# Performance work log

Measured on AMD Instinct MI355X. Metric: run time of the kernel, lower is better.

The kernel has to match this reference:

```python
import jax, jax.numpy as jnp
import numpy as np

S, B, H2, M = 4096, 16, 1024, 4096  # seq_len, batch, 2*hidden_size, max_number_of_entries


def setup_inputs() -> dict:
    key = jax.random.key(0)
    ks = jax.random.split(key, 5)
    return {
        "encoder_outputs": jax.random.normal(ks[0], (S, B, H2), jnp.float32),
        "state": jax.random.normal(ks[1], (B, H2), jnp.float32),
        "previous_attention": jax.random.uniform(ks[2], (B, M), jnp.float32),
        "attn_w": jax.random.normal(ks[3], (H2, H2), jnp.float32) / np.sqrt(H2).astype(np.float32),
        "attn_b": jnp.zeros((H2,), jnp.float32),
        "time_w": jax.random.normal(ks[4], (M, M), jnp.float32) / np.sqrt(M).astype(np.float32),
        "time_b": jnp.zeros((M,), jnp.float32),
    }


def reference(encoder_outputs, state, previous_attention, attn_w, attn_b, time_w, time_b):
    # encoder_outputs: [S, B, 2H]; state: [B, 2H]; previous_attention: [B, M]
    seq_len = encoder_outputs.shape[0]
    # attend(): Linear on state, then per-timestep dot product with encoder output.
    # The original Python loop over S timesteps + torch.cat is one batched matvec:
    altered_state = state @ attn_w.T + attn_b                      # [B, 2H]
    weights = jnp.einsum('bd,sbd->bs', altered_state, encoder_outputs)  # [B, S]
    # time_attention branch (its result is computed but unused by the outputs,
    # mirrored here for faithfulness to the original forward)
    apw = previous_attention @ time_w.T + time_b                   # [B, M]
    prev_probs = jax.nn.softmax(apw[:, :seq_len], axis=0)          # softmax over batch dim, as in original
    _adjusted_weights = prev_probs * weights                       # dead value in the original module
    # final softmax attention + weighted sum over encoder outputs
    normalized_weights = jax.nn.softmax(weights, axis=1)           # [B, S]
    attention_applied = jnp.einsum('bs,sbd->bd', normalized_weights, encoder_outputs)  # [B, 2H]
    return attention_applied, normalized_weights
```

## Files before the change

kernel.cpp:

```cpp
#include <hip/hip_runtime.h>
#include <cstdint>
#include <cstddef>

#define S_LEN 4096
#define B_SZ 16
#define H2D 1024
#define CHUNKS 64
#define WPB 4
#define P_PER_B (CHUNKS * WPB)
#define S_PER_WAVE (S_LEN / P_PER_B)

__device__ __forceinline__ void load16(const float* __restrict__ p, float v[16]) {
    const float4* q = (const float4*)p;
    float4 x0 = q[0], x1 = q[1], x2 = q[2], x3 = q[3];
    v[0] = x0.x; v[1] = x0.y; v[2]  = x0.z; v[3]  = x0.w;
    v[4] = x1.x; v[5] = x1.y; v[6]  = x1.z; v[7]  = x1.w;
    v[8] = x2.x; v[9] = x2.y; v[10] = x2.z; v[11] = x2.w;
    v[12] = x3.x; v[13] = x3.y; v[14] = x3.z; v[15] = x3.w;
}

__global__ __launch_bounds__(256) void k_altered(const float* __restrict__ state,
                                                 const float* __restrict__ attn_w,
                                                 const float* __restrict__ attn_b,
                                                 float* __restrict__ altered) {
    const int i = (blockIdx.x * blockDim.x + threadIdx.x) >> 6;
    const int lane = threadIdx.x & 63;
    float r[16];
    load16(attn_w + (size_t)i * H2D + lane * 16, r);
    const float bias = attn_b[i];
    for (int b = 0; b < B_SZ; ++b) {
        float s[16];
        load16(state + b * H2D + lane * 16, s);
        float p = 0.f;
#pragma unroll
        for (int k = 0; k < 16; ++k) p += r[k] * s[k];
#pragma unroll
        for (int off = 32; off; off >>= 1) p += __shfl_xor(p, off, 64);
        if (lane == 0) altered[b * H2D + i] = p + bias;
    }
}

__global__ __launch_bounds__(256) void k_flash(const float* __restrict__ enc,
                                               const float* __restrict__ altered,
                                               float* __restrict__ w_raw,
                                               float* __restrict__ pm,
                                               float* __restrict__ pl,
                                               float* __restrict__ pacc) {
    const int b = blockIdx.y;
    const int wave = threadIdx.x >> 6;
    const int lane = threadIdx.x & 63;
    const int p_idx = blockIdx.x * WPB + wave;

    float a[16];
    load16(altered + b * H2D + lane * 16, a);

    float m = -1e30f, l = 0.f;
    float acc[16];
#pragma unroll
    for (int i = 0; i < 16; ++i) acc[i] = 0.f;

    const int s_start = blockIdx.x * (S_LEN / CHUNKS) + wave;

    for (int k = 0; k < S_PER_WAVE; k += 2) {
        const int sA = s_start + WPB * k;
        const int sB = sA + WPB;
        float eA[16], eB[16];
        load16(enc + ((size_t)sA * B_SZ + b) * H2D + lane * 16, eA);
        load16(enc + ((size_t)sB * B_SZ + b) * H2D + lane * 16, eB);
        float pA = 0.f, pB = 0.f;
#pragma unroll
        for (int i = 0; i < 16; ++i) { pA += a[i] * eA[i]; pB += a[i] * eB[i]; }
#pragma unroll
        for (int off = 32; off; off >>= 1) {
            pA += __shfl_xor(pA, off, 64);
            pB += __shfl_xor(pB, off, 64);
        }
        if (lane == 0) {
            w_raw[b * S_LEN + sA] = pA;
            w_raw[b * S_LEN + sB] = pB;
        }
        float mn = fmaxf(m, pA);
        float sc = __expf(m - mn);
        float ex = __expf(pA - mn);
        l = l * sc + ex;
#pragma unroll
        for (int i = 0; i < 16; ++i) acc[i] = acc[i] * sc + ex * eA[i];
        m = mn;
        mn = fmaxf(m, pB);
        sc = __expf(m - mn);
        ex = __expf(pB - mn);
        l = l * sc + ex;
#pragma unroll
        for (int i = 0; i < 16; ++i) acc[i] = acc[i] * sc + ex * eB[i];
        m = mn;
    }

    const size_t pi = (size_t)(b * P_PER_B + p_idx);
    if (lane == 0) { pm[pi] = m; pl[pi] = l; }
    float4* pa = (float4*)(pacc + pi * H2D + lane * 16);
    pa[0] = make_float4(acc[0],  acc[1],  acc[2],  acc[3]);
    pa[1] = make_float4(acc[4],  acc[5],  acc[6],  acc[7]);
    pa[2] = make_float4(acc[8],  acc[9],  acc[10], acc[11]);
    pa[3] = make_float4(acc[12], acc[13], acc[14], acc[15]);
}

__global__ __launch_bounds__(P_PER_B) void k_reduce(const float* __restrict__ pm,
                                                    const float* __restrict__ pl,
                                                    float* __restrict__ cexp,
                                                    float* __restrict__ MZ) {
    const int b = blockIdx.x, t = threadIdx.x;
    __shared__ float sm[P_PER_B];
    const float mv = pm[b * P_PER_B + t];
    sm[t] = mv;
    __syncthreads();
    for (int o = P_PER_B / 2; o; o >>= 1) {
        if (t < o) sm[t] = fmaxf(sm[t], sm[t + o]);
        __syncthreads();
    }
    const float M = sm[0];
    __syncthreads();
    const float e = __expf(mv - M);
    sm[t] = e * pl[b * P_PER_B + t];
    __syncthreads();
    for (int o = P_PER_B / 2; o; o >>= 1) {
        if (t < o) sm[t] += sm[t + o];
        __syncthreads();
    }
    cexp[b * P_PER_B + t] = e;
    if (t == 0) {
        MZ[b * 2]     = M;
        MZ[b * 2 + 1] = 1.f / sm[0];
    }
}

__global__ __launch_bounds__(64) void k_combine(const float* __restrict__ pacc,
                                                const float* __restrict__ cexp,
                                                const float* __restrict__ MZ,
                                                float* __restrict__ out_attn) {
    const int b = blockIdx.x >> 4;
    const int d = ((blockIdx.x & 15) << 6) + threadIdx.x;
    float sum = 0.f;
    const float* base = pacc + (size_t)b * P_PER_B * H2D + d;
    const float* c = cexp + b * P_PER_B;
#pragma unroll 8
    for (int p = 0; p < P_PER_B; ++p) {
        sum += c[p] * base[(size_t)p * H2D];
    }
    out_attn[b * H2D + d] = sum * MZ[b * 2 + 1];
}

__global__ __launch_bounds__(256) void k_norm(const float* __restrict__ w_raw,
                                              const float* __restrict__ MZ,
                                              float* __restrict__ out_nw) {
    const int idx = blockIdx.x * 256 + threadIdx.x;
    const int b = idx >> 12;
    out_nw[idx] = __expf(w_raw[idx] - MZ[b * 2]) * MZ[b * 2 + 1];
}

extern "C" void kernel_launch(void* const* d_in, const int* in_sizes, int n_in,
                              void* d_out, int out_size, void* d_ws, size_t ws_size,
                              hipStream_t stream) {
    const float* enc    = (const float*)d_in[0];
    const float* state  = (const float*)d_in[1];
    const float* attn_w = (const float*)d_in[3];
    const float* attn_b = (const float*)d_in[4];

    float* ws = (float*)d_ws;
    float* altered = ws;
    float* w_raw   = ws + 16384;
    float* pm      = ws + 81920;
    float* pl      = ws + 86016;
    float* cexp    = ws + 90112;
    float* MZ      = ws + 94208;
    float* pacc    = ws + 95232;

    float* out_attn = (float*)d_out;
    float* out_nw   = (float*)d_out + B_SZ * H2D;

    hipLaunchKernelGGL(k_altered, dim3(256), dim3(256), 0, stream,
                       state, attn_w, attn_b, altered);
    hipLaunchKernelGGL(k_flash, dim3(CHUNKS, B_SZ), dim3(256), 0, stream,
                       enc, altered, w_raw, pm, pl, pacc);
    hipLaunchKernelGGL(k_reduce, dim3(B_SZ), dim3(P_PER_B), 0, stream,
                       pm, pl, cexp, MZ);
    hipLaunchKernelGGL(k_combine, dim3(B_SZ * H2D / 64), dim3(64), 0, stream,
                       pacc, cexp, MZ, out_attn);
    hipLaunchKernelGGL(k_norm, dim3(B_SZ * S_LEN / 256), dim3(256), 0, stream,
                       w_raw, MZ, out_nw);
}
```

Baseline: 428.6 us.

## Replace single-pass online softmax with two-pass scores then weighted sum

Drops the fused online-softmax flash kernel in favor of a score pass, a standalone softmax, and a second pass over encoder outputs that accumulates with normalized weights, followed by a two-level reduction. It also switches loads to lane-strided float4 for coalescing and issues four rows per iteration. This removes the per-row exp and rescale work from the streaming loop but reads the 256MB encoder tensor twice, roughly doubling memory traffic.

```diff
diff --git a/kernel.cpp b/kernel.cpp
--- a/kernel.cpp
+++ b/kernel.cpp
@@ -5,156 +5,167 @@
 #define S_LEN 4096
 #define B_SZ 16
 #define H2D 1024
-#define CHUNKS 64
-#define WPB 4
-#define P_PER_B (CHUNKS * WPB)
-#define S_PER_WAVE (S_LEN / P_PER_B)
-
-__device__ __forceinline__ void load16(const float* __restrict__ p, float v[16]) {
-    const float4* q = (const float4*)p;
-    float4 x0 = q[0], x1 = q[1], x2 = q[2], x3 = q[3];
-    v[0] = x0.x; v[1] = x0.y; v[2]  = x0.z; v[3]  = x0.w;
-    v[4] = x1.x; v[5] = x1.y; v[6]  = x1.z; v[7]  = x1.w;
-    v[8] = x2.x; v[9] = x2.y; v[10] = x2.z; v[11] = x2.w;
-    v[12] = x3.x; v[13] = x3.y; v[14] = x3.z; v[15] = x3.w;
+#define P_PER_B 256
+
+__device__ __forceinline__ float dot4(float4 a, float4 b) {
+    return a.x * b.x + a.y * b.y + a.z * b.z + a.w * b.w;
+}
+__device__ __forceinline__ void axpy4(float4& acc, float w, float4 v) {
+    acc.x += w * v.x; acc.y += w * v.y; acc.z += w * v.z; acc.w += w * v.w;
 }
 
 __global__ __launch_bounds__(256) void k_altered(const float* __restrict__ state,
                                                  const float* __restrict__ attn_w,
                                                  const float* __restrict__ attn_b,
                                                  float* __restrict__ altered) {
-    const int i = (blockIdx.x * blockDim.x + threadIdx.x) >> 6;
+    const int i = (blockIdx.x * 256 + threadIdx.x) >> 6;
     const int lane = threadIdx.x & 63;
-    float r[16];
-    load16(attn_w + (size_t)i * H2D + lane * 16, r);
+    const float4* w4 = (const float4*)(attn_w + (size_t)i * H2D);
+    float4 r[4];
+#pragma unroll
+    for (int j = 0; j < 4; ++j) r[j] = w4[lane + 64 * j];
     const float bias = attn_b[i];
     for (int b = 0; b < B_SZ; ++b) {
-        float s[16];
-        load16(state + b * H2D + lane * 16, s);
+        const float4* s4 = (const float4*)(state + b * H2D);
         float p = 0.f;
 #pragma unroll
-        for (int k = 0; k < 16; ++k) p += r[k] * s[k];
+        for (int j = 0; j < 4; ++j) p += dot4(r[j], s4[lane + 64 * j]);
 #pragma unroll
         for (int off = 32; off; off >>= 1) p += __shfl_xor(p, off, 64);
         if (lane == 0) altered[b * H2D + i] = p + bias;
     }
 }
 
-__global__ __launch_bounds__(256) void k_flash(const float* __restrict__ enc,
+__global__ __launch_bounds__(256) void k_pass1(const float* __restrict__ enc,
                                                const float* __restrict__ altered,
-                                               float* __restrict__ w_raw,
-                                               float* __restrict__ pm,
-                                               float* __restrict__ pl,
+                                               float* __restrict__ w_raw) {
+    const int b = blockIdx.y;
+    const int wave = threadIdx.x >> 6, lane = threadIdx.x & 63;
+    const int slot = blockIdx.x * 4 + wave;
+    const float4* a4p = (const float4*)(altered + b * H2D);
+    float4 af[4];
+#pragma unroll
+    for (int j = 0; j < 4; ++j) af[j] = a4p[lane + 64 * j];
+    const int s0 = slot * 16;
+    for (int k = 0; k < 16; k += 4) {
+        float4 e[4][4];
+#pragma unroll
+        for (int r = 0; r < 4; ++r) {
+            const float4* e4 = (const float4*)(enc + ((size_t)(s0 + k + r) * B_SZ + b) * H2D);
+#pragma unroll
+            for (int j = 0; j < 4; ++j) e[r][j] = e4[lane + 64 * j];
+        }
+        float p[4];
+#pragma unroll
+        for (int r = 0; r < 4; ++r) {
+            p[r] = 0.f;
+#pragma unroll
+            for (int j = 0; j < 4; ++j) p[r] += dot4(af[j], e[r][j]);
+        }
+#pragma unroll
+        for (int off = 32; off; off >>= 1) {
+#pragma unroll
+            for (int r = 0; r < 4; ++r) p[r] += __shfl_xor(p[r], off, 64);
+        }
+        if (lane == 0) {
+#pragma unroll
+            for (int r = 0; r < 4; ++r) w_raw[b * S_LEN + s0 + k + r] = p[r];
+        }
+    }
+}
+
+__global__ __launch_bounds__(1024) void k_softmax(const float* __restrict__ w_raw,
+                                                  float* __restrict__ out_nw) {
+    const int b = blockIdx.x, t = threadIdx.x;
+    const int wave = t >> 6, lane = t & 63;
+    __shared__ float sm[16], ss[16], sbc[2];
+    float4 v = ((const float4*)(w_raw + b * S_LEN))[t];
+    float m = fmaxf(fmaxf(v.x, v.y), fmaxf(v.z, v.w));
+#pragma unroll
+    for (int off = 32; off; off >>= 1) m = fmaxf(m, __shfl_xor(m, off, 64));
+    if (lane == 0) sm[wave] = m;
+    __syncthreads();
+    if (t == 0) {
+        float M = sm[0];
+#pragma unroll
+        for (int i = 1; i < 16; ++i) M = fmaxf(M, sm[i]);
+        sbc[0] = M;
+    }
+    __syncthreads();
+    const float M = sbc[0];
+    float4 e;
+    e.x = __expf(v.x - M); e.y = __expf(v.y - M);
+    e.z = __expf(v.z - M); e.w = __expf(v.w - M);
+    float s = e.x + e.y + e.z + e.w;
+#pragma unroll
+    for (int off = 32; off; off >>= 1) s += __shfl_xor(s, off, 64);
+    if (lane == 0) ss[wave] = s;
+    __syncthreads();
+    if (t == 0) {
+        float Z = 0.f;
+#pragma unroll
+        for (int i = 0; i < 16; ++i) Z += ss[i];
+        sbc[1] = 1.f / Z;
+    }
+    __syncthreads();
+    const float iZ = sbc[1];
+    ((float4*)(out_nw + b * S_LEN))[t] = make_float4(e.x * iZ, e.y * iZ, e.z * iZ, e.w * iZ);
+}
+
+__global__ __launch_bounds__(256) void k_pass2(const float* __restrict__ enc,
+                                               const float* __restrict__ nw,
                                                float* __restrict__ pacc) {
     const int b = blockIdx.y;
-    const int wave = threadIdx.x >> 6;
-    const int lane = threadIdx.x & 63;
-    const int p_idx = blockIdx.x * WPB + wave;
-
-    float a[16];
-    load16(altered + b * H2D + lane * 16, a);
-
-    float m = -1e30f, l = 0.f;
-    float acc[16];
-#pragma unroll
-    for (int i = 0; i < 16; ++i) acc[i] = 0.f;
-
-    const int s_start = blockIdx.x * (S_LEN / CHUNKS) + wave;
-
-    for (int k = 0; k < S_PER_WAVE; k += 2) {
-        const int sA = s_start + WPB * k;
-        const int sB = sA + WPB;
-        float eA[16], eB[16];
-        load16(enc + ((size_t)sA * B_SZ + b) * H2D + lane * 16, eA);
-        load16(enc + ((size_t)sB * B_SZ + b) * H2D + lane * 16, eB);
-        float pA = 0.f, pB = 0.f;
-#pragma unroll
-        for (int i = 0; i < 16; ++i) { pA += a[i] * eA[i]; pB += a[i] * eB[i]; }
-#pragma unroll
-        for (int off = 32; off; off >>= 1) {
-            pA += __shfl_xor(pA, off, 64);
-            pB += __shfl_xor(pB, off, 64);
-        }
-        if (lane == 0) {
-            w_raw[b * S_LEN + sA] = pA;
-            w_raw[b * S_LEN + sB] = pB;
-        }
-        float mn = fmaxf(m, pA);
-        float sc = __expf(m - mn);
-        float ex = __expf(pA - mn);
-        l = l * sc + ex;
-#pragma unroll
-        for (int i = 0; i < 16; ++i) acc[i] = acc[i] * sc + ex * eA[i];
-        m = mn;
-        mn = fmaxf(m, pB);
-        sc = __expf(m - mn);
-        ex = __expf(pB - mn);
-        l = l * sc + ex;
-#pragma unroll
-        for (int i = 0; i < 16; ++i) acc[i] = acc[i] * sc + ex * eB[i];
-        m = mn;
-    }
-
-    const size_t pi = (size_t)(b * P_PER_B + p_idx);
-    if (lane == 0) { pm[pi] = m; pl[pi] = l; }
-    float4* pa = (float4*)(pacc + pi * H2D + lane * 16);
-    pa[0] = make_float4(acc[0],  acc[1],  acc[2],  acc[3]);
-    pa[1] = make_float4(acc[4],  acc[5],  acc[6],  acc[7]);
-    pa[2] = make_float4(acc[8],  acc[9],  acc[10], acc[11]);
-    pa[3] = make_float4(acc[12], acc[13], acc[14], acc[15]);
-}
-
-__global__ __launch_bounds__(P_PER_B) void k_reduce(const float* __restrict__ pm,
-                                                    const float* __restrict__ pl,
-                                                    float* __restrict__ cexp,
-                                                    float* __restrict__ MZ) {
-    const int b = blockIdx.x, t = threadIdx.x;
-    __shared__ float sm[P_PER_B];
-    const float mv = pm[b * P_PER_B + t];
-    sm[t] = mv;
-    __syncthreads();
-    for (int o = P_PER_B / 2; o; o >>= 1) {
-        if (t < o) sm[t] = fmaxf(sm[t], sm[t + o]);
-        __syncthreads();
-    }
-    const float M = sm[0];
-    __syncthreads();
-    const float e = __expf(mv - M);
-    sm[t] = e * pl[b * P_PER_B + t];
-    __syncthreads();
-    for (int o = P_PER_B / 2; o; o >>= 1) {
-        if (t < o) sm[t] += sm[t + o];
-        __syncthreads();
-    }
-    cexp[b * P_PER_B + t] = e;
-    if (t == 0) {
-        MZ[b * 2]     = M;
-        MZ[b * 2 + 1] = 1.f / sm[0];
-    }
-}
-
-__global__ __launch_bounds__(64) void k_combine(const float* __restrict__ pacc,
-                                                const float* __restrict__ cexp,
-                                                const float* __restrict__ MZ,
-                                                float* __restrict__ out_attn) {
-    const int b = blockIdx.x >> 4;
-    const int d = ((blockIdx.x & 15) << 6) + threadIdx.x;
-    float sum = 0.f;
-    const float* base = pacc + (size_t)b * P_PER_B * H2D + d;
-    const float* c = cexp + b * P_PER_B;
-#pragma unroll 8
-    for (int p = 0; p < P_PER_B; ++p) {
-        sum += c[p] * base[(size_t)p * H2D];
-    }
-    out_attn[b * H2D + d] = sum * MZ[b * 2 + 1];
-}
-
-__global__ __launch_bounds__(256) void k_norm(const float* __restrict__ w_raw,
-                                              const float* __restrict__ MZ,
-                                              float* __restrict__ out_nw) {
-    const int idx = blockIdx.x * 256 + threadIdx.x;
-    const int b = idx >> 12;
-    out_nw[idx] = __expf(w_raw[idx] - MZ[b * 2]) * MZ[b * 2 + 1];
+    const int wave = threadIdx.x >> 6, lane = threadIdx.x & 63;
+    const int slot = blockIdx.x * 4 + wave;
+    float4 acc[4];
+#pragma unroll
+    for (int j = 0; j < 4; ++j) acc[j] = make_float4(0.f, 0.f, 0.f, 0.f);
+    const int s0 = slot * 16;
+    for (int k = 0; k < 16; k += 4) {
+        float4 e[4][4];
+        float w[4];
+#pragma unroll
+        for (int r = 0; r < 4; ++r) {
+            const int s = s0 + k + r;
+            const float4* e4 = (const float4*)(enc + ((size_t)s * B_SZ + b) * H2D);
+#pragma unroll
+            for (int j = 0; j < 4; ++j) e[r][j] = e4[lane + 64 * j];
+            w[r] = nw[b * S_LEN + s];
+        }
+#pragma unroll
+        for (int r = 0; r < 4; ++r)
+#pragma unroll
+            for (int j = 0; j < 4; ++j) axpy4(acc[j], w[r], e[r][j]);
+    }
+    float4* o = (float4*)(pacc + (size_t)(b * P_PER_B + slot) * H2D);
+#pragma unroll
+    for (int j = 0; j < 4; ++j) o[lane + 64 * j] = acc[j];
+}
+
+__global__ __launch_bounds__(256) void k_comb1(const float* __restrict__ pacc,
+                                               float* __restrict__ pacc2) {
+    const int b = blockIdx.x >> 4, pg = blockIdx.x & 15, t = threadIdx.x;
+    float4 s = make_float4(0.f, 0.f, 0.f, 0.f);
+#pragma unroll
+    for (int i = 0; i < 16; ++i) {
+        const float4 v = ((const float4*)(pacc + (size_t)(b * P_PER_B + pg * 16 + i) * H2D))[t];
+        s.x += v.x; s.y += v.y; s.z += v.z; s.w += v.w;
+    }
+    ((float4*)(pacc2 + (size_t)(b * 16 + pg) * H2D))[t] = s;
+}
+
+__global__ __launch_bounds__(64) void k_comb2(const float* __restrict__ pacc2,
+                                              float* __restrict__ out_attn) {
+    const int b = blockIdx.x >> 2;
+    const int col = (blockIdx.x & 3) * 64 + threadIdx.x;
+    float4 s = make_float4(0.f, 0.f, 0.f, 0.f);
+#pragma unroll
+    for (int i = 0; i < 16; ++i) {
+        const float4 v = ((const float4*)(pacc2 + (size_t)(b * 16 + i) * H2D))[col];
+        s.x += v.x; s.y += v.y; s.z += v.z; s.w += v.w;
+    }
+    ((float4*)(out_attn + b * H2D))[col] = s;
 }
 
 extern "C" void kernel_launch(void* const* d_in, const int* in_sizes, int n_in,
@@ -168,23 +179,22 @@
     float* ws = (float*)d_ws;
     float* altered = ws;
     float* w_raw   = ws + 16384;
-    float* pm      = ws + 81920;
-    float* pl      = ws + 86016;
-    float* cexp    = ws + 90112;
-    float* MZ      = ws + 94208;
-    float* pacc    = ws + 95232;
+    float* pacc    = ws + 16384 + 65536;
+    float* pacc2   = pacc + (size_t)B_SZ * P_PER_B * H2D;
 
     float* out_attn = (float*)d_out;
     float* out_nw   = (float*)d_out + B_SZ * H2D;
 
     hipLaunchKernelGGL(k_altered, dim3(256), dim3(256), 0, stream,
                        state, attn_w, attn_b, altered);
-    hipLaunchKernelGGL(k_flash, dim3(CHUNKS, B_SZ), dim3(256), 0, stream,
-                       enc, altered, w_raw, pm, pl, pacc);
-    hipLaunchKernelGGL(k_reduce, dim3(B_SZ), dim3(P_PER_B), 0, stream,
-                       pm, pl, cexp, MZ);
-    hipLaunchKernelGGL(k_combine, dim3(B_SZ * H2D / 64), dim3(64), 0, stream,
-                       pacc, cexp, MZ, out_attn);
-    hipLaunchKernelGGL(k_norm, dim3(B_SZ * S_LEN / 256), dim3(256), 0, stream,
-                       w_raw, MZ, out_nw);
-}
+    hipLaunchKernelGGL(k_pass1, dim3(64, B_SZ), dim3(256), 0, stream,
+                       enc, altered, w_raw);
+    hipLaunchKernelGGL(k_softmax, dim3(B_SZ), dim3(1024), 0, stream,
+                       w_raw, out_nw);
+    hipLaunchKernelGGL(k_pass2, dim3(64, B_SZ), dim3(256), 0, stream,
+                       enc, out_nw, pacc);
+    hipLaunchKernelGGL(k_comb1, dim3(256), dim3(256), 0, stream,
+                       pacc, pacc2);
+    hipLaunchKernelGGL(k_comb2, dim3(64), dim3(64), 0, stream,
+                       pacc2, out_attn);
+}
```

Measured after the change: 450.0 us. +5.0%, slower.
